# Kernel tuning notes

Hardware: AMD Instinct MI355X
Metric: run time of the kernel (lower is better)

## Reference

```python
import jax, jax.numpy as jnp
import numpy as np
from jax import lax

WINDOW_SIZE = 11
SIGMA = 1.5
DATA_RANGE = 2.0


def _gauss_1d(size, sigma):
    coords = np.arange(size, dtype=np.float32) - size // 2
    g = np.exp(-coords ** 2 / (2.0 * sigma ** 2))
    g /= g.sum()
    return jnp.asarray(g)


def _gaussian_filter_2d(x, window):
    # x: (N, C, H, W); separable depthwise Gaussian blur
    C = x.shape[1]
    pad = window.shape[0] // 2
    win_h = jnp.tile(window.reshape(1, 1, 1, -1), (C, 1, 1, 1))  # (C,1,1,K)
    win_v = jnp.tile(window.reshape(1, 1, -1, 1), (C, 1, 1, 1))  # (C,1,K,1)
    dn = ('NCHW', 'OIHW', 'NCHW')
    out = lax.conv_general_dilated(x, win_h, window_strides=(1, 1),
                                   padding=((0, 0), (pad, pad)),
                                   dimension_numbers=dn, feature_group_count=C)
    out = lax.conv_general_dilated(out, win_v, window_strides=(1, 1),
                                   padding=((pad, pad), (0, 0)),
                                   dimension_numbers=dn, feature_group_count=C)
    return out


def _ssim_2d(x, y):
    C1 = (0.01 * DATA_RANGE) ** 2
    C2 = (0.03 * DATA_RANGE) ** 2
    window = _gauss_1d(WINDOW_SIZE, SIGMA).astype(x.dtype)
    mu_x = _gaussian_filter_2d(x, window)
    mu_y = _gaussian_filter_2d(y, window)
    mu_x_sq = mu_x * mu_x
    mu_y_sq = mu_y * mu_y
    mu_xy = mu_x * mu_y
    sigma_x_sq = jnp.maximum(_gaussian_filter_2d(x * x, window) - mu_x_sq, 0.0)
    sigma_y_sq = jnp.maximum(_gaussian_filter_2d(y * y, window) - mu_y_sq, 0.0)
    sigma_xy = _gaussian_filter_2d(x * y, window) - mu_xy
    ssim_map = ((2.0 * mu_xy + C1) * (2.0 * sigma_xy + C2)) / (
        (mu_x_sq + mu_y_sq + C1) * (sigma_x_sq + sigma_y_sq + C2))
    return ssim_map.mean()


def setup_inputs() -> dict:
    key = jax.random.key(0)
    k1, k2 = jax.random.split(key)
    pred = jax.random.normal(k1, (16, 3, 512, 512), dtype=jnp.float32)
    target = jax.random.normal(k2, (16, 3, 512, 512), dtype=jnp.float32)
    return {"pred": pred, "target": target}


def reference(pred, target):
    return 1.0 - _ssim_2d(pred, target)
```

## Files before the change

### kernel.cpp

```cpp
#include <hip/hip_runtime.h>
#include <math.h>


typedef _Float16 f16x8 __attribute__((ext_vector_type(8)));
typedef _Float16 f16x4 __attribute__((ext_vector_type(4)));
typedef float f32x4 __attribute__((ext_vector_type(4)));
typedef _Float16 h2 __attribute__((ext_vector_type(2)));

#if __has_builtin(__builtin_amdgcn_mfma_f32_16x16x16_f16)
#define MFMA16 __builtin_amdgcn_mfma_f32_16x16x16_f16
#else
#define MFMA16 __builtin_amdgcn_mfma_f32_16x16x16f16
#endif

#define RAWP 88
#define NPIX (16 * 3 * 512 * 512)
#define NBLOCKS (48 * 16 * 8)

union U4 { f16x4 v; h2 p[2]; };
union U8 { f16x8 v; h2 p[4]; };
union UP { h2 h; unsigned u; };
union UB2 { unsigned u[2]; f16x4 v; };

static __device__ __forceinline__ h2 pkrtz(float a, float b) {
    auto r = __builtin_amdgcn_cvt_pkrtz(a, b);
    union { decltype(r) f; h2 h; } x; x.f = r; return x.h;
}
static __device__ __forceinline__ unsigned pk_u32(float a, float b) {
    UP x; x.h = pkrtz(a, b); return x.u;
}

struct alignas(16) BandTabs { float bh[64][8]; float wa0[64][4]; float wa16[64][4]; };
static constexpr BandTabs mk_tabs() {
    constexpr float GW[11] = {
        0.00102838f, 0.00759876f, 0.03600026f, 0.10936083f, 0.21300567f,
        0.26601190f, 0.21300567f, 0.10936083f, 0.03600026f, 0.00759876f,
        0.00102838f};
    BandTabs t{};
    for (int lane = 0; lane < 64; ++lane) {
        const int l15 = lane & 15, kg = lane >> 4;
        for (int j = 0; j < 8; ++j) {
            const int ib = (kg * 8 + j) - l15 - 3;
            t.bh[lane][j] = (ib >= 0 && ib < 11) ? GW[ib] : 0.0f;
        }
        for (int j = 0; j < 4; ++j) {
            const int kl = 4 * kg + j;
            const int i0 = kl - l15;
            const int i1 = 16 + kl - l15;
            t.wa0[lane][j]  = (i0 >= 0 && i0 < 11) ? GW[i0] : 0.0f;
            t.wa16[lane][j] = (i1 >= 0 && i1 < 11) ? GW[i1] : 0.0f;
        }
    }
    return t;
}
__device__ constexpr BandTabs TAB = mk_tabs();

static __device__ __forceinline__ f16x8 load_band8(const float* row) {
    const float4 a = *(const float4*)row;
    const float4 b = *(const float4*)(row + 4);
    U8 r;
    r.p[0] = pkrtz(a.x, a.y); r.p[1] = pkrtz(a.z, a.w);
    r.p[2] = pkrtz(b.x, b.y); r.p[3] = pkrtz(b.z, b.w);
    return r.v;
}
static __device__ __forceinline__ f16x4 load_band4(const float* row) {
    const float4 a = *(const float4*)row;
    U4 r;
    r.p[0] = pkrtz(a.x, a.y); r.p[1] = pkrtz(a.z, a.w);
    return r.v;
}

__global__ __launch_bounds__(256, 8) void ssim_main(
    const float* __restrict__ X, const float* __restrict__ Y,
    float* __restrict__ partial)
{
    __shared__ _Float16 rawx[48 * RAWP];
    __shared__ _Float16 rawy[48 * RAWP];
    __shared__ float red[4];

    const int tid = threadIdx.x;
    const int bid = blockIdx.x;

    const int wg    = (bid & 7) * (NBLOCKS / 8) + (bid >> 3);
    const int plane = wg >> 7;
    const int tt    = wg & 127;
    const int tr    = tt >> 3;
    const int tc    = tt & 7;

    const float* xp = X + (size_t)plane * (512 * 512);
    const float* yp = Y + (size_t)plane * (512 * 512);
    const int row0 = tr * 32 - 5;
    const int colT = tc * 64;
    const int colB = colT - 8;

    for (int u = tid; u < 960; u += 256) {
        const int r  = u / 20;
        const int c4 = u - r * 20;
        const int gr = row0 + r;
        const int gc = colB + 4 * c4;
        const bool ok = ((unsigned)gr < 512u) && ((unsigned)gc <= 508u);
        float4 xv = make_float4(0.f, 0.f, 0.f, 0.f), yv = xv;
        if (ok) {
            xv = *(const float4*)(xp + gr * 512 + gc);
            yv = *(const float4*)(yp + gr * 512 + gc);
        }
        U4 tx, ty;
        tx.p[0] = pkrtz(xv.x, xv.y); tx.p[1] = pkrtz(xv.z, xv.w);
        ty.p[0] = pkrtz(yv.x, yv.y); ty.p[1] = pkrtz(yv.z, yv.w);
        *(f16x4*)(rawx + r * RAWP + 4 * c4) = tx.v;
        *(f16x4*)(rawy + r * RAWP + 4 * c4) = ty.v;
    }

    const int w    = tid >> 6;
    const int lane = tid & 63;
    const int l15  = lane & 15;
    const int kg   = lane >> 4;

    const f16x8 BH   = load_band8(TAB.bh[lane]);
    const f16x4 WVA0 = load_band4(TAB.wa0[lane]);
    const f16x4 WVA16= load_band4(TAB.wa16[lane]);

    __syncthreads();

    const f32x4 zero4 = {0.f, 0.f, 0.f, 0.f};
    const int rawc = 16 * w + 8 * kg;

    unsigned pq[4][3][2];
#pragma unroll
    for (int mt = 0; mt < 3; ++mt) {
        const int r = mt * 16 + l15;
        const f16x8 fx = *(const f16x8*)(rawx + r * RAWP + rawc);
        const f16x8 fy = *(const f16x8*)(rawy + r * RAWP + rawc);
        const f16x8 fxy = fx * fy;
        const f16x8 fss = fx * fx + fy * fy;

        const f32x4 c0 = __builtin_amdgcn_mfma_f32_16x16x32_f16(fx,  BH, zero4, 0, 0, 0);
        const f32x4 c1 = __builtin_amdgcn_mfma_f32_16x16x32_f16(fy,  BH, zero4, 0, 0, 0);
        const f32x4 c2 = __builtin_amdgcn_mfma_f32_16x16x32_f16(fss, BH, zero4, 0, 0, 0);
        const f32x4 c3 = __builtin_amdgcn_mfma_f32_16x16x32_f16(fxy, BH, zero4, 0, 0, 0);

        pq[0][mt][0] = pk_u32(c0[0], c0[1]); pq[0][mt][1] = pk_u32(c0[2], c0[3]);
        pq[1][mt][0] = pk_u32(c1[0], c1[1]); pq[1][mt][1] = pk_u32(c1[2], c1[3]);
        pq[2][mt][0] = pk_u32(c2[0], c2[1]); pq[2][mt][1] = pk_u32(c2[2], c2[3]);
        pq[3][mt][0] = pk_u32(c3[0], c3[1]); pq[3][mt][1] = pk_u32(c3[2], c3[3]);
    }

    const float C1 = 0.0004f, C2 = 0.0036f;
    float lsum = 0.f;
#pragma unroll
    for (int mtv = 0; mtv < 2; ++mtv) {
        f32x4 v[4];
#pragma unroll
        for (int q = 0; q < 4; ++q) {
            UB2 blo, bhi;
            blo.u[0] = pq[q][mtv][0];     blo.u[1] = pq[q][mtv][1];
            bhi.u[0] = pq[q][mtv + 1][0]; bhi.u[1] = pq[q][mtv + 1][1];
            f32x4 acc = MFMA16(WVA16, bhi.v, zero4, 0, 0, 0);
            v[q] = MFMA16(WVA0, blo.v, acc, 0, 0, 0);
        }
#pragma unroll
        for (int r2 = 0; r2 < 4; ++r2) {
            const float mux = v[0][r2], muy = v[1][r2];
            const float ess = v[2][r2], exy = v[3][r2];
            const float mux2 = mux * mux, muy2 = muy * muy, muxy = mux * muy;
            const float svar = fmaxf(ess - mux2 - muy2, 0.f);
            const float sxy = exy - muxy;
            const float num = (2.f * muxy + C1) * (2.f * sxy + C2);
            const float den = (mux2 + muy2 + C1) * (svar + C2);
            lsum += num * __builtin_amdgcn_rcpf(den);
        }
    }

#pragma unroll
    for (int off = 32; off > 0; off >>= 1)
        lsum += __shfl_down(lsum, off, 64);
    if (lane == 0) red[w] = lsum;
    __syncthreads();
    if (tid == 0)
        partial[bid] = red[0] + red[1] + red[2] + red[3];
}

__global__ void ssim_final(const float* __restrict__ partial,
                           float* __restrict__ out)
{
    const int tid = threadIdx.x;
    double s = 0.0;
    for (int i = tid; i < NBLOCKS; i += 1024) s += (double)partial[i];
#pragma unroll
    for (int off = 32; off > 0; off >>= 1)
        s += __shfl_down(s, off, 64);
    __shared__ double ws[16];
    if ((tid & 63) == 0) ws[tid >> 6] = s;
    __syncthreads();
    if (tid == 0) {
        double tot = 0.0;
#pragma unroll
        for (int i = 0; i < 16; ++i) tot += ws[i];
        out[0] = (float)(1.0 - tot / (double)NPIX);
    }
}

extern "C" void kernel_launch(void* const* d_in, const int* in_sizes, int n_in,
                              void* d_out, int out_size, void* d_ws, size_t ws_size,
                              hipStream_t stream)
{
    const float* x = (const float*)d_in[0];
    const float* y = (const float*)d_in[1];
    float* partial = (float*)d_ws;
    float* out = (float*)d_out;

    ssim_main<<<NBLOCKS, 256, 0, stream>>>(x, y, partial);
    ssim_final<<<1, 1024, 0, stream>>>(partial, out);
}
```

Baseline: 33.11 us.

## Persistent blocks with double-buffered tile prefetch and fused last-block reduction

```diff
diff --git a/kernel.cpp b/kernel.cpp
--- a/kernel.cpp
+++ b/kernel.cpp
@@ -15,7 +15,8 @@
 
 #define RAWP 88
 #define NPIX (16 * 3 * 512 * 512)
-#define NBLOCKS (48 * 16 * 8)
+#define NBLK 2048
+#define TILES 6144
 
 union U4 { f16x4 v; h2 p[2]; };
 union U8 { f16x8 v; h2 p[4]; };
@@ -70,104 +71,129 @@
     return r.v;
 }
 
-__global__ __launch_bounds__(256, 8) void ssim_main(
+__global__ __launch_bounds__(256, 4) void ssim_fused(
     const float* __restrict__ X, const float* __restrict__ Y,
-    float* __restrict__ partial)
+    float* __restrict__ partial, unsigned* __restrict__ counter,
+    float* __restrict__ out)
 {
-    __shared__ _Float16 rawx[48 * RAWP];
-    __shared__ _Float16 rawy[48 * RAWP];
+    __shared__ _Float16 raw[2][2][48 * RAWP];
     __shared__ float red[4];
+    __shared__ int lastFlag;
+    __shared__ double ws2[4];
 
     const int tid = threadIdx.x;
     const int bid = blockIdx.x;
-
-    const int wg    = (bid & 7) * (NBLOCKS / 8) + (bid >> 3);
-    const int plane = wg >> 7;
-    const int tt    = wg & 127;
-    const int tr    = tt >> 3;
-    const int tc    = tt & 7;
-
-    const float* xp = X + (size_t)plane * (512 * 512);
-    const float* yp = Y + (size_t)plane * (512 * 512);
-    const int row0 = tr * 32 - 5;
-    const int colT = tc * 64;
-    const int colB = colT - 8;
-
-    for (int u = tid; u < 960; u += 256) {
-        const int r  = u / 20;
-        const int c4 = u - r * 20;
-        const int gr = row0 + r;
-        const int gc = colB + 4 * c4;
-        const bool ok = ((unsigned)gr < 512u) && ((unsigned)gc <= 508u);
-        float4 xv = make_float4(0.f, 0.f, 0.f, 0.f), yv = xv;
-        if (ok) {
-            xv = *(const float4*)(xp + gr * 512 + gc);
-            yv = *(const float4*)(yp + gr * 512 + gc);
-        }
-        U4 tx, ty;
-        tx.p[0] = pkrtz(xv.x, xv.y); tx.p[1] = pkrtz(xv.z, xv.w);
-        ty.p[0] = pkrtz(yv.x, yv.y); ty.p[1] = pkrtz(yv.z, yv.w);
-        *(f16x4*)(rawx + r * RAWP + 4 * c4) = tx.v;
-        *(f16x4*)(rawy + r * RAWP + 4 * c4) = ty.v;
-    }
 
     const int w    = tid >> 6;
     const int lane = tid & 63;
     const int l15  = lane & 15;
     const int kg   = lane >> 4;
 
-    const f16x8 BH   = load_band8(TAB.bh[lane]);
-    const f16x4 WVA0 = load_band4(TAB.wa0[lane]);
-    const f16x4 WVA16= load_band4(TAB.wa16[lane]);
-
-    __syncthreads();
+    int ru_[4], c4_[4]; bool uok_[4];
+#pragma unroll
+    for (int i = 0; i < 4; ++i) {
+        const int u = tid + 256 * i;
+        ru_[i] = u / 20;
+        c4_[i] = u - ru_[i] * 20;
+        uok_[i] = (u < 960);
+    }
+
+    const f16x8 BH    = load_band8(TAB.bh[lane]);
+    const f16x4 WVA0  = load_band4(TAB.wa0[lane]);
+    const f16x4 WVA16 = load_band4(TAB.wa16[lane]);
 
     const f32x4 zero4 = {0.f, 0.f, 0.f, 0.f};
+    const float4 f4z = make_float4(0.f, 0.f, 0.f, 0.f);
     const int rawc = 16 * w + 8 * kg;
-
-    unsigned pq[4][3][2];
-#pragma unroll
-    for (int mt = 0; mt < 3; ++mt) {
-        const int r = mt * 16 + l15;
-        const f16x8 fx = *(const f16x8*)(rawx + r * RAWP + rawc);
-        const f16x8 fy = *(const f16x8*)(rawy + r * RAWP + rawc);
-        const f16x8 fxy = fx * fy;
-        const f16x8 fss = fx * fx + fy * fy;
-
-        const f32x4 c0 = __builtin_amdgcn_mfma_f32_16x16x32_f16(fx,  BH, zero4, 0, 0, 0);
-        const f32x4 c1 = __builtin_amdgcn_mfma_f32_16x16x32_f16(fy,  BH, zero4, 0, 0, 0);
-        const f32x4 c2 = __builtin_amdgcn_mfma_f32_16x16x32_f16(fss, BH, zero4, 0, 0, 0);
-        const f32x4 c3 = __builtin_amdgcn_mfma_f32_16x16x32_f16(fxy, BH, zero4, 0, 0, 0);
-
-        pq[0][mt][0] = pk_u32(c0[0], c0[1]); pq[0][mt][1] = pk_u32(c0[2], c0[3]);
-        pq[1][mt][0] = pk_u32(c1[0], c1[1]); pq[1][mt][1] = pk_u32(c1[2], c1[3]);
-        pq[2][mt][0] = pk_u32(c2[0], c2[1]); pq[2][mt][1] = pk_u32(c2[2], c2[3]);
-        pq[3][mt][0] = pk_u32(c3[0], c3[1]); pq[3][mt][1] = pk_u32(c3[2], c3[3]);
-    }
-
     const float C1 = 0.0004f, C2 = 0.0036f;
     float lsum = 0.f;
-#pragma unroll
-    for (int mtv = 0; mtv < 2; ++mtv) {
-        f32x4 v[4];
-#pragma unroll
-        for (int q = 0; q < 4; ++q) {
-            UB2 blo, bhi;
-            blo.u[0] = pq[q][mtv][0];     blo.u[1] = pq[q][mtv][1];
-            bhi.u[0] = pq[q][mtv + 1][0]; bhi.u[1] = pq[q][mtv + 1][1];
-            f32x4 acc = MFMA16(WVA16, bhi.v, zero4, 0, 0, 0);
-            v[q] = MFMA16(WVA0, blo.v, acc, 0, 0, 0);
-        }
-#pragma unroll
-        for (int r2 = 0; r2 < 4; ++r2) {
-            const float mux = v[0][r2], muy = v[1][r2];
-            const float ess = v[2][r2], exy = v[3][r2];
-            const float mux2 = mux * mux, muy2 = muy * muy, muxy = mux * muy;
-            const float svar = fmaxf(ess - mux2 - muy2, 0.f);
-            const float sxy = exy - muxy;
-            const float num = (2.f * muxy + C1) * (2.f * sxy + C2);
-            const float den = (mux2 + muy2 + C1) * (svar + C2);
-            lsum += num * __builtin_amdgcn_rcpf(den);
+    float4 px[4], py[4];
+
+    auto issue = [&](int k) {
+        const int g   = k * NBLK + bid;
+        const int wgk = (g & 7) * (TILES / 8) + (g >> 3);
+        const int pl  = wgk >> 7;
+        const int tt  = wgk & 127;
+        const int tr  = tt >> 3;
+        const int tc  = tt & 7;
+        const float* xp = X + (size_t)pl * (512 * 512);
+        const float* yp = Y + (size_t)pl * (512 * 512);
+        const int row0 = tr * 32 - 5;
+        const int colB = tc * 64 - 8;
+#pragma unroll
+        for (int i = 0; i < 4; ++i) {
+            const int gr = row0 + ru_[i];
+            const int gc = colB + 4 * c4_[i];
+            const bool ok = uok_[i] && ((unsigned)gr < 512u) && ((unsigned)gc <= 508u);
+            px[i] = ok ? *(const float4*)(xp + gr * 512 + gc) : f4z;
+            py[i] = ok ? *(const float4*)(yp + gr * 512 + gc) : f4z;
+        }
+    };
+
+    issue(0);
+
+#pragma unroll
+    for (int k = 0; k < 3; ++k) {
+        const int buf = k & 1;
+        _Float16* rx = raw[buf][0];
+        _Float16* ry = raw[buf][1];
+#pragma unroll
+        for (int i = 0; i < 4; ++i) {
+            if (uok_[i]) {
+                const int off = ru_[i] * RAWP + 4 * c4_[i];
+                U4 tx, ty;
+                tx.p[0] = pkrtz(px[i].x, px[i].y); tx.p[1] = pkrtz(px[i].z, px[i].w);
+                ty.p[0] = pkrtz(py[i].x, py[i].y); ty.p[1] = pkrtz(py[i].z, py[i].w);
+                *(f16x4*)(rx + off) = tx.v;
+                *(f16x4*)(ry + off) = ty.v;
+            }
+        }
+        __syncthreads();
+
+        if (k < 2) issue(k + 1);
+
+        unsigned pq[4][3][2];
+#pragma unroll
+        for (int mt = 0; mt < 3; ++mt) {
+            const int r = mt * 16 + l15;
+            const f16x8 fx = *(const f16x8*)(rx + r * RAWP + rawc);
+            const f16x8 fy = *(const f16x8*)(ry + r * RAWP + rawc);
+            const f16x8 fxy = fx * fy;
+            const f16x8 fss = fx * fx + fy * fy;
+
+            const f32x4 c0 = __builtin_amdgcn_mfma_f32_16x16x32_f16(fx,  BH, zero4, 0, 0, 0);
+            const f32x4 c1 = __builtin_amdgcn_mfma_f32_16x16x32_f16(fy,  BH, zero4, 0, 0, 0);
+            const f32x4 c2 = __builtin_amdgcn_mfma_f32_16x16x32_f16(fss, BH, zero4, 0, 0, 0);
+            const f32x4 c3 = __builtin_amdgcn_mfma_f32_16x16x32_f16(fxy, BH, zero4, 0, 0, 0);
+
+            pq[0][mt][0] = pk_u32(c0[0], c0[1]); pq[0][mt][1] = pk_u32(c0[2], c0[3]);
+            pq[1][mt][0] = pk_u32(c1[0], c1[1]); pq[1][mt][1] = pk_u32(c1[2], c1[3]);
+            pq[2][mt][0] = pk_u32(c2[0], c2[1]); pq[2][mt][1] = pk_u32(c2[2], c2[3]);
+            pq[3][mt][0] = pk_u32(c3[0], c3[1]); pq[3][mt][1] = pk_u32(c3[2], c3[3]);
+        }
+
+#pragma unroll
+        for (int mtv = 0; mtv < 2; ++mtv) {
+            f32x4 v[4];
+#pragma unroll
+            for (int q = 0; q < 4; ++q) {
+                UB2 blo, bhi;
+                blo.u[0] = pq[q][mtv][0];     blo.u[1] = pq[q][mtv][1];
+                bhi.u[0] = pq[q][mtv + 1][0]; bhi.u[1] = pq[q][mtv + 1][1];
+                f32x4 acc = MFMA16(WVA16, bhi.v, zero4, 0, 0, 0);
+                v[q] = MFMA16(WVA0, blo.v, acc, 0, 0, 0);
+            }
+#pragma unroll
+            for (int r2 = 0; r2 < 4; ++r2) {
+                const float mux = v[0][r2], muy = v[1][r2];
+                const float ess = v[2][r2], exy = v[3][r2];
+                const float mux2 = mux * mux, muy2 = muy * muy, muxy = mux * muy;
+                const float svar = fmaxf(ess - mux2 - muy2, 0.f);
+                const float sxy = exy - muxy;
+                const float num = (2.f * muxy + C1) * (2.f * sxy + C2);
+                const float den = (mux2 + muy2 + C1) * (svar + C2);
+                lsum += num * __builtin_amdgcn_rcpf(den);
+            }
         }
     }
 
@@ -176,27 +202,28 @@
         lsum += __shfl_down(lsum, off, 64);
     if (lane == 0) red[w] = lsum;
     __syncthreads();
-    if (tid == 0)
+    if (tid == 0) {
         partial[bid] = red[0] + red[1] + red[2] + red[3];
-}
-
-__global__ void ssim_final(const float* __restrict__ partial,
-                           float* __restrict__ out)
-{
-    const int tid = threadIdx.x;
-    double s = 0.0;
-    for (int i = tid; i < NBLOCKS; i += 1024) s += (double)partial[i];
-#pragma unroll
-    for (int off = 32; off > 0; off >>= 1)
-        s += __shfl_down(s, off, 64);
-    __shared__ double ws[16];
-    if ((tid & 63) == 0) ws[tid >> 6] = s;
+        __threadfence();
+        const unsigned old = atomicAdd(counter, 1u);
+        lastFlag = (old == NBLK - 1);
+    }
     __syncthreads();
-    if (tid == 0) {
-        double tot = 0.0;
-#pragma unroll
-        for (int i = 0; i < 16; ++i) tot += ws[i];
-        out[0] = (float)(1.0 - tot / (double)NPIX);
+
+    if (lastFlag) {
+        double s = 0.0;
+#pragma unroll
+        for (int j = 0; j < 8; ++j)
+            s += (double)atomicAdd(&partial[tid * 8 + j], 0.0f);
+#pragma unroll
+        for (int off = 32; off > 0; off >>= 1)
+            s += __shfl_down(s, off, 64);
+        if (lane == 0) ws2[w] = s;
+        __syncthreads();
+        if (tid == 0) {
+            const double tot = ws2[0] + ws2[1] + ws2[2] + ws2[3];
+            out[0] = (float)(1.0 - tot / (double)NPIX);
+        }
     }
 }
 
@@ -207,8 +234,9 @@
     const float* x = (const float*)d_in[0];
     const float* y = (const float*)d_in[1];
     float* partial = (float*)d_ws;
+    unsigned* counter = (unsigned*)((char*)d_ws + NBLK * 4);
     float* out = (float*)d_out;
 
-    ssim_main<<<NBLOCKS, 256, 0, stream>>>(x, y, partial);
-    ssim_final<<<1, 1024, 0, stream>>>(partial, out);
-}
+    hipMemsetAsync(counter, 0, sizeof(unsigned), stream);
+    ssim_fused<<<NBLK, 256, 0, stream>>>(x, y, partial, counter, out);
+}
```

Result: slower. 106.5 us (+221.8%).
